# Optimization experiments

Measured on AMD Instinct MI355X. Metric: run time of the kernel, lower is better.

Reference implementation:

```python
import jax, jax.numpy as jnp
import numpy as np

# Perfect-tree regularization of the recursive UpDownVec graph:
#   T tactics per internal node, S siblings per tactic, L levels, branching B = T*S.
T, S, L = 2, 4, 7
B = T * S
DIM = 128
EPS = 1.0  # epsilon in AggChildrenVec
SIZES = [B ** l for l in range(L)]          # nodes per level: 1, 8, ..., 262144
OFFS = np.concatenate([[0], np.cumsum(SIZES)])
N_TOTAL = int(OFFS[-1])                      # 299593


def setup_inputs() -> dict:
    key = jax.random.key(0)
    ks = jax.random.split(key, 12)
    sc = 1.0 / np.sqrt(DIM)
    return {
        "initial_vecs": jax.random.normal(ks[0], (N_TOTAL, DIM), jnp.float32),
        "Ws": jax.random.normal(ks[1], (DIM, DIM), jnp.float32) * sc,
        "bs": jax.random.normal(ks[2], (DIM,), jnp.float32) * sc,
        "Wc": jax.random.normal(ks[3], (DIM, DIM), jnp.float32) * sc,
        "bc": jax.random.normal(ks[4], (DIM,), jnp.float32) * sc,
        "Wx": jax.random.normal(ks[5], (DIM, DIM), jnp.float32) * sc,
        "bx": jax.random.normal(ks[6], (DIM,), jnp.float32) * sc,
        "Wf": jax.random.normal(ks[7], (DIM, 2 * DIM), jnp.float32) * sc,
        "bf": jax.random.normal(ks[8], (DIM,), jnp.float32) * sc,
        "Wh": jax.random.normal(ks[9], (1, DIM), jnp.float32) * sc,
        "bh": jax.random.normal(ks[10], (1,), jnp.float32) * sc,
    }


def reference(initial_vecs, Ws, bs, Wc, bc, Wx, bx, Wf, bf, Wh, bh):
    dim = initial_vecs.shape[-1]
    init = [initial_vecs[OFFS[l]:OFFS[l + 1]] for l in range(L)]  # static slices

    # ---- up_step (bottom-up): leaves -> root ----
    agg = [None] * L
    agg[L - 1] = init[L - 1]                                    # leaves: agg = initial
    for l in range(L - 2, -1, -1):
        ch = agg[l + 1].reshape(SIZES[l], T, S, dim)            # children agg vecs
        # AggSiblingsVec: mean over siblings of relu(linear)
        sib_h = jax.nn.relu(jnp.einsum('ntsd,ed->ntse', ch, Ws) + bs)
        sib_agg = sib_h.mean(axis=2)                            # [n, T, dim]
        # AggChildrenVec: node + eps * mean over tactics of relu(linear)
        ch_h = jax.nn.relu(jnp.einsum('ntd,ed->nte', sib_agg, Wc) + bc)
        agg[l] = init[l] + EPS * ch_h.mean(axis=1)

    # ---- down_step (top-down): root -> leaves ----
    ctx = [None] * L
    ctx[0] = jnp.ones((1, dim), initial_vecs.dtype)             # root context = ones
    for l in range(L - 1):
        # AggContextVec over cat([parent_ctx, other_siblings_agg]); mean is
        # order-invariant so set-based sibling gathering is reproduced exactly.
        h = jax.nn.relu(agg[l + 1] @ Wx.T + bx).reshape(SIZES[l], T, S, dim)
        sum_h = h.sum(axis=2)                                   # [n, T, dim]
        ctx_h = jax.nn.relu(ctx[l] @ Wx.T + bx)                 # [n, dim]
        child_ctx = (ctx_h[:, None, None, :] + sum_h[:, :, None, :] - h) / S
        ctx[l + 1] = child_ctx.reshape(SIZES[l + 1], dim)

    # ---- final_agg for every node ----
    ctx_all = jnp.concatenate(ctx, axis=0)                      # [N, dim]
    agg_all = jnp.concatenate(agg, axis=0)                      # [N, dim]
    x = jnp.concatenate([ctx_all, agg_all], axis=1)             # [N, 2*dim]
    x = jax.nn.relu(x @ Wf.T + bf)
    return x @ Wh.T + bh                                        # [N, 1]
```

## Files before the change

kernel.cpp:

```cpp
#include <hip/hip_runtime.h>
#include <stdint.h>

#define DIM 128
#define LPAD 136

static constexpr long long NTOT = 299593LL;

using bf16x8 = __attribute__((ext_vector_type(8))) __bf16;
using f32x4  = __attribute__((ext_vector_type(4))) float;

__device__ __forceinline__ float relu(float x){ return x > 0.f ? x : 0.f; }
__device__ __forceinline__ __bf16 tobf(float x){ return (__bf16)x; }

__device__ __forceinline__ void mfma_acc(f32x4& acc, bf16x8 a, bf16x8 b){
    acc = __builtin_amdgcn_mfma_f32_16x16x32_bf16(a, b, acc, 0, 0, 0);
}

__device__ __forceinline__ void load_w_lds(const __bf16* __restrict__ wsrc,
                                           __bf16* lds, int src_stride){
    int t = threadIdx.x;
    #pragma unroll
    for (int i = 0; i < 8; ++i){
        int idx = t + i*256;
        int row = idx >> 4, col8 = (idx & 15) << 3;
        *(uint4*)(&lds[row*LPAD + col8]) = *(const uint4*)(wsrc + row*src_stride + col8);
    }
}

__global__ __launch_bounds__(256) void prep_kernel(
    const float* __restrict__ Ws, const float* __restrict__ Wc,
    const float* __restrict__ Wx, const float* __restrict__ Wf,
    __bf16* __restrict__ wts, __bf16* __restrict__ ctx)
{
    int idx = blockIdx.x*256 + threadIdx.x;
    if      (idx < 16384) wts[idx] = tobf(Ws[idx]);
    else if (idx < 32768) wts[idx] = tobf(Wc[idx - 16384]);
    else if (idx < 49152) wts[idx] = tobf(Wx[idx - 32768]);
    else if (idx < 81920) wts[idx] = tobf(Wf[idx - 49152]);
    else if (idx < 82048) ctx[idx - 81920] = tobf(1.0f);
}

template<bool LEAF>
__global__ __launch_bounds__(256, 3) void up_kernel(
    const __bf16* __restrict__ wts,
    const float* __restrict__ init,
    const float* __restrict__ bs, const float* __restrict__ bc,
    __bf16* __restrict__ agg,
    long long child_base, long long parent_base, long long n_par)
{
    __shared__ __bf16 lds_w[128*LPAD];
    __shared__ __bf16 lds_sib[32*LPAD];

    const int t = threadIdx.x;
    const int w = t >> 6, lane = t & 63, quad = lane >> 4, l15 = lane & 15;

    load_w_lds(wts, lds_w, 128);
    __syncthreads();

    const long long n_child = n_par * 8;
    const long long rowbase = (long long)blockIdx.x*128 + w*32;

    f32x4 acc[2][8];
    #pragma unroll
    for (int tt = 0; tt < 2; ++tt)
        #pragma unroll
        for (int i = 0; i < 8; ++i) acc[tt][i] = f32x4{0.f,0.f,0.f,0.f};

    bf16x8 af[2][4];
    #pragma unroll
    for (int tt = 0; tt < 2; ++tt){
        long long r = rowbase + tt*16 + l15;
        if (r >= n_child) r = n_child - 1;
        const long long base = (child_base + r)*DIM;
        #pragma unroll
        for (int ks = 0; ks < 4; ++ks){
            if (LEAF){
                const float* p = init + base + ks*32 + quad*8;
                float4 v0 = *(const float4*)p;
                float4 v1 = *(const float4*)(p + 4);
                bf16x8 a;
                a[0]=tobf(v0.x); a[1]=tobf(v0.y); a[2]=tobf(v0.z); a[3]=tobf(v0.w);
                a[4]=tobf(v1.x); a[5]=tobf(v1.y); a[6]=tobf(v1.z); a[7]=tobf(v1.w);
                af[tt][ks] = a;
                *(uint4*)(agg + base + ks*32 + quad*8) = *(uint4*)&a;
            } else {
                af[tt][ks] = *(const bf16x8*)(agg + base + ks*32 + quad*8);
            }
        }
    }
    #pragma unroll
    for (int ks = 0; ks < 4; ++ks){
        #pragma unroll
        for (int nt = 0; nt < 8; ++nt){
            bf16x8 bfrag = *(const bf16x8*)&lds_w[(nt*16 + l15)*LPAD + ks*32 + quad*8];
            mfma_acc(acc[0][nt], af[0][ks], bfrag);
            mfma_acc(acc[1][nt], af[1][ks], bfrag);
        }
    }
    #pragma unroll
    for (int tt = 0; tt < 2; ++tt){
        const int g = w*8 + tt*4 + quad;
        #pragma unroll
        for (int nt = 0; nt < 8; ++nt){
            int col = nt*16 + l15;
            float b = bs[col];
            float s = relu(acc[tt][nt][0]+b) + relu(acc[tt][nt][1]+b)
                    + relu(acc[tt][nt][2]+b) + relu(acc[tt][nt][3]+b);
            lds_sib[g*LPAD + col] = tobf(s * 0.25f);
        }
    }
    __syncthreads();
    load_w_lds(wts + 16384, lds_w, 128);
    __syncthreads();

    if (w < 2){
        f32x4 a2c[8];
        #pragma unroll
        for (int i = 0; i < 8; ++i) a2c[i] = f32x4{0.f,0.f,0.f,0.f};
        bf16x8 a2[4];
        #pragma unroll
        for (int ks = 0; ks < 4; ++ks)
            a2[ks] = *(const bf16x8*)&lds_sib[(w*16 + l15)*LPAD + ks*32 + quad*8];
        #pragma unroll
        for (int ks = 0; ks < 4; ++ks){
            #pragma unroll
            for (int nt = 0; nt < 8; ++nt){
                bf16x8 bfrag = *(const bf16x8*)&lds_w[(nt*16 + l15)*LPAD + ks*32 + quad*8];
                mfma_acc(a2c[nt], a2[ks], bfrag);
            }
        }
        const long long p0 = (long long)blockIdx.x*16 + w*8 + quad*2;
        const long long p1 = p0 + 1;
        #pragma unroll
        for (int nt = 0; nt < 8; ++nt){
            int col = nt*16 + l15;
            float b = bc[col];
            float r0 = relu(a2c[nt][0]+b), r1 = relu(a2c[nt][1]+b);
            float r2 = relu(a2c[nt][2]+b), r3 = relu(a2c[nt][3]+b);
            if (p0 < n_par){
                long long gr = parent_base + p0;
                agg[gr*DIM + col] = tobf(init[gr*DIM + col] + 0.5f*(r0+r1));
            }
            if (p1 < n_par){
                long long gr = parent_base + p1;
                agg[gr*DIM + col] = tobf(init[gr*DIM + col] + 0.5f*(r2+r3));
            }
        }
    }
}

__global__ __launch_bounds__(256, 3) void down_kernel(
    const __bf16* __restrict__ wts,
    const float* __restrict__ bx,
    const __bf16* __restrict__ agg,
    __bf16* __restrict__ ctx,
    long long parent_base, long long child_base, long long n_par)
{
    __shared__ __bf16 lds_w[128*LPAD];
    __shared__ float lds_ctxh[16*132];

    const int t = threadIdx.x;
    const int w = t >> 6, lane = t & 63, quad = lane >> 4, l15 = lane & 15;

    load_w_lds(wts + 32768, lds_w, 128);
    __syncthreads();

    const long long n_child = n_par*8;

    if (w == 0){
        f32x4 acc[8];
        #pragma unroll
        for (int i = 0; i < 8; ++i) acc[i] = f32x4{0.f,0.f,0.f,0.f};
        bf16x8 a[4];
        long long p = (long long)blockIdx.x*16 + l15;
        if (p >= n_par) p = n_par - 1;
        #pragma unroll
        for (int ks = 0; ks < 4; ++ks)
            a[ks] = *(const bf16x8*)(ctx + (parent_base + p)*DIM + ks*32 + quad*8);
        #pragma unroll
        for (int ks = 0; ks < 4; ++ks){
            #pragma unroll
            for (int nt = 0; nt < 8; ++nt){
                bf16x8 bfrag = *(const bf16x8*)&lds_w[(nt*16 + l15)*LPAD + ks*32 + quad*8];
                mfma_acc(acc[nt], a[ks], bfrag);
            }
        }
        #pragma unroll
        for (int nt = 0; nt < 8; ++nt){
            int col = nt*16 + l15;
            float b = bx[col];
            #pragma unroll
            for (int rg = 0; rg < 4; ++rg)
                lds_ctxh[(quad*4 + rg)*132 + col] = relu(acc[nt][rg] + b);
        }
    }
    __syncthreads();

    f32x4 acc[2][8];
    #pragma unroll
    for (int tt = 0; tt < 2; ++tt)
        #pragma unroll
        for (int i = 0; i < 8; ++i) acc[tt][i] = f32x4{0.f,0.f,0.f,0.f};
    bf16x8 a[2][4];
    const long long rowbase = (long long)blockIdx.x*128 + w*32;
    #pragma unroll
    for (int tt = 0; tt < 2; ++tt){
        long long r = rowbase + tt*16 + l15;
        if (r >= n_child) r = n_child - 1;
        #pragma unroll
        for (int ks = 0; ks < 4; ++ks)
            a[tt][ks] = *(const bf16x8*)(agg + (child_base + r)*DIM + ks*32 + quad*8);
    }
    #pragma unroll
    for (int ks = 0; ks < 4; ++ks){
        #pragma unroll
        for (int nt = 0; nt < 8; ++nt){
            bf16x8 bfrag = *(const bf16x8*)&lds_w[(nt*16 + l15)*LPAD + ks*32 + quad*8];
            mfma_acc(acc[0][nt], a[0][ks], bfrag);
            mfma_acc(acc[1][nt], a[1][ks], bfrag);
        }
    }
    #pragma unroll
    for (int tt = 0; tt < 2; ++tt){
        const long long rb = rowbase + tt*16 + quad*4;
        const int p_loc = w*4 + tt*2 + (quad >> 1);
        #pragma unroll
        for (int nt = 0; nt < 8; ++nt){
            int col = nt*16 + l15;
            float b = bx[col];
            float h0 = relu(acc[tt][nt][0]+b), h1 = relu(acc[tt][nt][1]+b);
            float h2 = relu(acc[tt][nt][2]+b), h3 = relu(acc[tt][nt][3]+b);
            float s = h0 + h1 + h2 + h3;
            float ch = lds_ctxh[p_loc*132 + col];
            if (rb   < n_child) ctx[(child_base + rb  )*DIM + col] = tobf((ch + s - h0)*0.25f);
            if (rb+1 < n_child) ctx[(child_base + rb+1)*DIM + col] = tobf((ch + s - h1)*0.25f);
            if (rb+2 < n_child) ctx[(child_base + rb+2)*DIM + col] = tobf((ch + s - h2)*0.25f);
            if (rb+3 < n_child) ctx[(child_base + rb+3)*DIM + col] = tobf((ch + s - h3)*0.25f);
        }
    }
}

__global__ __launch_bounds__(256, 3) void final_kernel(
    const __bf16* __restrict__ wts,
    const __bf16* __restrict__ ctx,
    const __bf16* __restrict__ agg,
    const float* __restrict__ bf_,
    const float* __restrict__ Wh, const float* __restrict__ bh,
    float* __restrict__ out)
{
    __shared__ __bf16 lds_w[128*LPAD];
    const int t = threadIdx.x;
    const int w = t >> 6, lane = t & 63, quad = lane >> 4, l15 = lane & 15;

    f32x4 acc[2][8];
    #pragma unroll
    for (int tt = 0; tt < 2; ++tt)
        #pragma unroll
        for (int i = 0; i < 8; ++i) acc[tt][i] = f32x4{0.f,0.f,0.f,0.f};

    const long long rowbase = (long long)blockIdx.x*128 + w*32;

    #pragma unroll
    for (int half = 0; half < 2; ++half){
        load_w_lds(wts + 49152 + half*128, lds_w, 256);
        __syncthreads();
        const __bf16* src = half ? agg : ctx;
        bf16x8 a[2][4];
        #pragma unroll
        for (int tt = 0; tt < 2; ++tt){
            long long r = rowbase + tt*16 + l15;
            if (r >= NTOT) r = NTOT - 1;
            #pragma unroll
            for (int ks = 0; ks < 4; ++ks)
                a[tt][ks] = *(const bf16x8*)(src + r*DIM + ks*32 + quad*8);
        }
        #pragma unroll
        for (int ks = 0; ks < 4; ++ks){
            #pragma unroll
            for (int nt = 0; nt < 8; ++nt){
                bf16x8 bfrag = *(const bf16x8*)&lds_w[(nt*16 + l15)*LPAD + ks*32 + quad*8];
                mfma_acc(acc[0][nt], a[0][ks], bfrag);
                mfma_acc(acc[1][nt], a[1][ks], bfrag);
            }
        }
        __syncthreads();
    }

    #pragma unroll
    for (int tt = 0; tt < 2; ++tt){
        float p0 = 0.f, p1 = 0.f, p2 = 0.f, p3 = 0.f;
        #pragma unroll
        for (int nt = 0; nt < 8; ++nt){
            int col = nt*16 + l15;
            float b = bf_[col], wh = Wh[col];
            p0 += relu(acc[tt][nt][0]+b)*wh;
            p1 += relu(acc[tt][nt][1]+b)*wh;
            p2 += relu(acc[tt][nt][2]+b)*wh;
            p3 += relu(acc[tt][nt][3]+b)*wh;
        }
        #pragma unroll
        for (int m = 1; m < 16; m <<= 1){
            p0 += __shfl_xor(p0, m);
            p1 += __shfl_xor(p1, m);
            p2 += __shfl_xor(p2, m);
            p3 += __shfl_xor(p3, m);
        }
        if (l15 == 0){
            float bb = bh[0];
            long long r = rowbase + tt*16 + quad*4;
            if (r   < NTOT) out[r  ] = p0 + bb;
            if (r+1 < NTOT) out[r+1] = p1 + bb;
            if (r+2 < NTOT) out[r+2] = p2 + bb;
            if (r+3 < NTOT) out[r+3] = p3 + bb;
        }
    }
}

extern "C" void kernel_launch(void* const* d_in, const int* in_sizes, int n_in,
                              void* d_out, int out_size, void* d_ws, size_t ws_size,
                              hipStream_t stream)
{
    const float* init = (const float*)d_in[0];
    const float* Ws  = (const float*)d_in[1];
    const float* bs  = (const float*)d_in[2];
    const float* Wc  = (const float*)d_in[3];
    const float* bc  = (const float*)d_in[4];
    const float* Wx  = (const float*)d_in[5];
    const float* bx  = (const float*)d_in[6];
    const float* Wf  = (const float*)d_in[7];
    const float* bff = (const float*)d_in[8];
    const float* Wh  = (const float*)d_in[9];
    const float* bh  = (const float*)d_in[10];
    float* out = (float*)d_out;

    __bf16* agg = (__bf16*)d_ws;
    __bf16* ctx = agg + NTOT*DIM;
    __bf16* wts = ctx + NTOT*DIM;

    static const long long SZ[7] = {1,8,64,512,4096,32768,262144};
    static const long long OF[8] = {0,1,9,73,585,4681,37449,299593};

    prep_kernel<<<dim3(321), dim3(256), 0, stream>>>(Ws, Wc, Wx, Wf, wts, ctx);

    for (int l = 5; l >= 0; --l){
        int blocks = (int)((SZ[l]*8 + 127)/128);
        if (l == 5)
            up_kernel<true><<<dim3(blocks), dim3(256), 0, stream>>>(
                wts, init, bs, bc, agg, OF[6], OF[5], SZ[5]);
        else
            up_kernel<false><<<dim3(blocks), dim3(256), 0, stream>>>(
                wts, init, bs, bc, agg, OF[l+1], OF[l], SZ[l]);
    }
    for (int l = 0; l < 6; ++l){
        int blocks = (int)((SZ[l]*8 + 127)/128);
        down_kernel<<<dim3(blocks), dim3(256), 0, stream>>>(
            wts, bx, agg, ctx, OF[l], OF[l+1], SZ[l]);
    }
    final_kernel<<<dim3((int)((NTOT + 127)/128)), dim3(256), 0, stream>>>(
        wts, ctx, agg, bff, Wh, bh, out);
}
```

Measured before the change: 422.2 us.

## Split large-level up/down passes and prelayout weights in MFMA fragment order

Weights are pre-permuted into MFMA B-fragment order so each lane reads a contiguous 16-byte chunk from LDS without padding. The bottom level's up pass is split into a sibling-aggregation kernel and a tactic kernel that go through a scratch buffer. The leaf-level down pass is split into a parent context-transform kernel and a child kernel. The final projection now uses 512-thread blocks that hold both weight halves in LDS and loop over two tiles, which removes the mid-kernel reload and sync. This adds extra launches and intermediate global traffic (sib, ctxh) in exchange for better-parallelized large levels and cheaper LDS access.

```diff
diff --git a/kernel.cpp b/kernel.cpp
--- a/kernel.cpp
+++ b/kernel.cpp
@@ -27,21 +27,366 @@
     }
 }
 
+template<int NTHR>
+__device__ __forceinline__ void stage_fm(const __bf16* __restrict__ src, __bf16* lds){
+    const int t = threadIdx.x;
+    #pragma unroll
+    for (int i = 0; i < 2048/NTHR; ++i){
+        int c = i*NTHR + t;
+        *((uint4*)lds + c) = *((const uint4*)src + c);
+    }
+}
+
 __global__ __launch_bounds__(256) void prep_kernel(
     const float* __restrict__ Ws, const float* __restrict__ Wc,
     const float* __restrict__ Wx, const float* __restrict__ Wf,
     __bf16* __restrict__ wts, __bf16* __restrict__ ctx)
 {
     int idx = blockIdx.x*256 + threadIdx.x;
-    if      (idx < 16384) wts[idx] = tobf(Ws[idx]);
-    else if (idx < 32768) wts[idx] = tobf(Wc[idx - 16384]);
-    else if (idx < 49152) wts[idx] = tobf(Wx[idx - 32768]);
-    else if (idx < 81920) wts[idx] = tobf(Wf[idx - 49152]);
-    else if (idx < 82048) ctx[idx - 81920] = tobf(1.0f);
-}
-
-template<bool LEAF>
-__global__ __launch_bounds__(256, 3) void up_kernel(
+    if (idx < 81920){
+        float v;
+        if      (idx < 16384) v = Ws[idx];
+        else if (idx < 32768) v = Wc[idx - 16384];
+        else if (idx < 49152) v = Wx[idx - 32768];
+        else                  v = Wf[idx - 49152];
+        wts[idx] = tobf(v);
+    } else if (idx < 163840){
+        int d2 = idx - 81920;
+        int sel = d2 >> 14;
+        int d   = d2 & 16383;
+        int j = d & 7, ln = (d >> 3) & 63, f = d >> 9;
+        int r = (f >> 2)*16 + (ln & 15);
+        int c = (f & 3)*32 + (ln >> 4)*8 + j;
+        float v;
+        if      (sel == 0) v = Ws[r*128 + c];
+        else if (sel == 1) v = Wc[r*128 + c];
+        else if (sel == 2) v = Wx[r*128 + c];
+        else if (sel == 3) v = Wf[r*256 + c];
+        else               v = Wf[r*256 + 128 + c];
+        wts[idx] = tobf(v);
+    } else if (idx < 163968){
+        ctx[idx - 163840] = tobf(1.0f);
+    }
+}
+
+
+__global__ __launch_bounds__(256, 4) void up1_kernel(
+    const __bf16* __restrict__ wfm, const float* __restrict__ init,
+    const float* __restrict__ bs, __bf16* __restrict__ agg,
+    __bf16* __restrict__ sib, long long child_base)
+{
+    __shared__ __attribute__((aligned(16))) __bf16 lds_w[16384];
+    stage_fm<256>(wfm, lds_w);
+    __syncthreads();
+    const int t = threadIdx.x, w = t>>6, lane = t&63, quad = lane>>4, l15 = lane&15;
+    float bsr[8];
+    #pragma unroll
+    for (int nt = 0; nt < 8; ++nt) bsr[nt] = bs[nt*16 + l15];
+    const int gw = blockIdx.x*4 + w;
+    #pragma unroll 1
+    for (int k = 0; k < 2; ++k){
+        const long long tile = gw + k*4096;
+        const long long r0 = tile*32;
+        float4 v[2][4][2];
+        #pragma unroll
+        for (int tt = 0; tt < 2; ++tt){
+            const float* p = init + (child_base + r0 + tt*16 + l15)*DIM + quad*8;
+            #pragma unroll
+            for (int ks = 0; ks < 4; ++ks){
+                v[tt][ks][0] = *(const float4*)(p + ks*32);
+                v[tt][ks][1] = *(const float4*)(p + ks*32 + 4);
+            }
+        }
+        bf16x8 af[2][4];
+        #pragma unroll
+        for (int tt = 0; tt < 2; ++tt){
+            const long long ob = (child_base + r0 + tt*16 + l15)*DIM + quad*8;
+            #pragma unroll
+            for (int ks = 0; ks < 4; ++ks){
+                bf16x8 a;
+                a[0]=tobf(v[tt][ks][0].x); a[1]=tobf(v[tt][ks][0].y);
+                a[2]=tobf(v[tt][ks][0].z); a[3]=tobf(v[tt][ks][0].w);
+                a[4]=tobf(v[tt][ks][1].x); a[5]=tobf(v[tt][ks][1].y);
+                a[6]=tobf(v[tt][ks][1].z); a[7]=tobf(v[tt][ks][1].w);
+                af[tt][ks] = a;
+                *(uint4*)(agg + ob + ks*32) = *(uint4*)&a;
+            }
+        }
+        f32x4 acc[2][8];
+        #pragma unroll
+        for (int tt = 0; tt < 2; ++tt)
+            #pragma unroll
+            for (int i = 0; i < 8; ++i) acc[tt][i] = f32x4{0.f,0.f,0.f,0.f};
+        #pragma unroll
+        for (int ks = 0; ks < 4; ++ks){
+            #pragma unroll
+            for (int nt = 0; nt < 8; ++nt){
+                bf16x8 b = *(const bf16x8*)&lds_w[((nt*4+ks)<<9) + lane*8];
+                mfma_acc(acc[0][nt], af[0][ks], b);
+                mfma_acc(acc[1][nt], af[1][ks], b);
+            }
+        }
+        #pragma unroll
+        for (int tt = 0; tt < 2; ++tt){
+            const long long g = tile*8 + tt*4 + quad;
+            #pragma unroll
+            for (int nt = 0; nt < 8; ++nt){
+                float b = bsr[nt];
+                float s = relu(acc[tt][nt][0]+b) + relu(acc[tt][nt][1]+b)
+                        + relu(acc[tt][nt][2]+b) + relu(acc[tt][nt][3]+b);
+                sib[g*DIM + nt*16 + l15] = tobf(s*0.25f);
+            }
+        }
+    }
+}
+
+__global__ __launch_bounds__(256, 4) void up2_kernel(
+    const __bf16* __restrict__ wfm, const float* __restrict__ init,
+    const float* __restrict__ bc, const __bf16* __restrict__ sib,
+    __bf16* __restrict__ agg, long long parent_base)
+{
+    __shared__ __attribute__((aligned(16))) __bf16 lds_w[16384];
+    stage_fm<256>(wfm, lds_w);
+    __syncthreads();
+    const int t = threadIdx.x, w = t>>6, lane = t&63, quad = lane>>4, l15 = lane&15;
+    float bcr[8];
+    #pragma unroll
+    for (int nt = 0; nt < 8; ++nt) bcr[nt] = bc[nt*16 + l15];
+    const int gw = blockIdx.x*4 + w;
+    const long long r0 = (long long)gw*32;
+    bf16x8 a[2][4];
+    #pragma unroll
+    for (int tt = 0; tt < 2; ++tt)
+        #pragma unroll
+        for (int ks = 0; ks < 4; ++ks)
+            a[tt][ks] = *(const bf16x8*)(sib + (r0 + tt*16 + l15)*DIM + ks*32 + quad*8);
+    f32x4 acc[2][8];
+    #pragma unroll
+    for (int tt = 0; tt < 2; ++tt)
+        #pragma unroll
+        for (int i = 0; i < 8; ++i) acc[tt][i] = f32x4{0.f,0.f,0.f,0.f};
+    #pragma unroll
+    for (int ks = 0; ks < 4; ++ks){
+        #pragma unroll
+        for (int nt = 0; nt < 8; ++nt){
+            bf16x8 b = *(const bf16x8*)&lds_w[((nt*4+ks)<<9) + lane*8];
+            mfma_acc(acc[0][nt], a[0][ks], b);
+            mfma_acc(acc[1][nt], a[1][ks], b);
+        }
+    }
+    #pragma unroll
+    for (int tt = 0; tt < 2; ++tt){
+        const long long p0 = r0/2 + tt*8 + quad*2;
+        const long long p1 = p0 + 1;
+        #pragma unroll
+        for (int nt = 0; nt < 8; ++nt){
+            int col = nt*16 + l15;
+            float b = bcr[nt];
+            float r0_ = relu(acc[tt][nt][0]+b), r1_ = relu(acc[tt][nt][1]+b);
+            float r2_ = relu(acc[tt][nt][2]+b), r3_ = relu(acc[tt][nt][3]+b);
+            long long gr0 = parent_base + p0, gr1 = parent_base + p1;
+            agg[gr0*DIM + col] = tobf(init[gr0*DIM + col] + 0.5f*(r0_+r1_));
+            agg[gr1*DIM + col] = tobf(init[gr1*DIM + col] + 0.5f*(r2_+r3_));
+        }
+    }
+}
+
+__global__ __launch_bounds__(256, 4) void downh_kernel(
+    const __bf16* __restrict__ wfm, const float* __restrict__ bx,
+    const __bf16* __restrict__ ctx, __bf16* __restrict__ ctxh,
+    long long parent_base)
+{
+    __shared__ __attribute__((aligned(16))) __bf16 lds_w[16384];
+    stage_fm<256>(wfm, lds_w);
+    __syncthreads();
+    const int t = threadIdx.x, w = t>>6, lane = t&63, quad = lane>>4, l15 = lane&15;
+    float bxr[8];
+    #pragma unroll
+    for (int nt = 0; nt < 8; ++nt) bxr[nt] = bx[nt*16 + l15];
+    const int gw = blockIdx.x*4 + w;
+    const long long r0 = (long long)gw*32;
+    bf16x8 a[2][4];
+    #pragma unroll
+    for (int tt = 0; tt < 2; ++tt)
+        #pragma unroll
+        for (int ks = 0; ks < 4; ++ks)
+            a[tt][ks] = *(const bf16x8*)(ctx + (parent_base + r0 + tt*16 + l15)*DIM + ks*32 + quad*8);
+    f32x4 acc[2][8];
+    #pragma unroll
+    for (int tt = 0; tt < 2; ++tt)
+        #pragma unroll
+        for (int i = 0; i < 8; ++i) acc[tt][i] = f32x4{0.f,0.f,0.f,0.f};
+    #pragma unroll
+    for (int ks = 0; ks < 4; ++ks){
+        #pragma unroll
+        for (int nt = 0; nt < 8; ++nt){
+            bf16x8 b = *(const bf16x8*)&lds_w[((nt*4+ks)<<9) + lane*8];
+            mfma_acc(acc[0][nt], a[0][ks], b);
+            mfma_acc(acc[1][nt], a[1][ks], b);
+        }
+    }
+    #pragma unroll
+    for (int tt = 0; tt < 2; ++tt){
+        #pragma unroll
+        for (int nt = 0; nt < 8; ++nt){
+            int col = nt*16 + l15;
+            float b = bxr[nt];
+            #pragma unroll
+            for (int rg = 0; rg < 4; ++rg){
+                long long row = r0 + tt*16 + quad*4 + rg;
+                ctxh[row*DIM + col] = tobf(relu(acc[tt][nt][rg] + b));
+            }
+        }
+    }
+}
+
+__global__ __launch_bounds__(256, 4) void downc_kernel(
+    const __bf16* __restrict__ wfm, const float* __restrict__ bx,
+    const __bf16* __restrict__ agg, const __bf16* __restrict__ ctxh,
+    __bf16* __restrict__ ctx, long long child_base)
+{
+    __shared__ __attribute__((aligned(16))) __bf16 lds_w[16384];
+    stage_fm<256>(wfm, lds_w);
+    __syncthreads();
+    const int t = threadIdx.x, w = t>>6, lane = t&63, quad = lane>>4, l15 = lane&15;
+    float bxr[8];
+    #pragma unroll
+    for (int nt = 0; nt < 8; ++nt) bxr[nt] = bx[nt*16 + l15];
+    const int gw = blockIdx.x*4 + w;
+    #pragma unroll 1
+    for (int k = 0; k < 2; ++k){
+        const long long tile = gw + k*4096;
+        const long long r0 = tile*32;
+        bf16x8 a[2][4];
+        #pragma unroll
+        for (int tt = 0; tt < 2; ++tt)
+            #pragma unroll
+            for (int ks = 0; ks < 4; ++ks)
+                a[tt][ks] = *(const bf16x8*)(agg + (child_base + r0 + tt*16 + l15)*DIM + ks*32 + quad*8);
+        f32x4 acc[2][8];
+        #pragma unroll
+        for (int tt = 0; tt < 2; ++tt)
+            #pragma unroll
+            for (int i = 0; i < 8; ++i) acc[tt][i] = f32x4{0.f,0.f,0.f,0.f};
+        #pragma unroll
+        for (int ks = 0; ks < 4; ++ks){
+            #pragma unroll
+            for (int nt = 0; nt < 8; ++nt){
+                bf16x8 b = *(const bf16x8*)&lds_w[((nt*4+ks)<<9) + lane*8];
+                mfma_acc(acc[0][nt], a[0][ks], b);
+                mfma_acc(acc[1][nt], a[1][ks], b);
+            }
+        }
+        #pragma unroll
+        for (int tt = 0; tt < 2; ++tt){
+            const long long rb = r0 + tt*16 + quad*4;
+            const long long p  = rb >> 3;
+            #pragma unroll
+            for (int nt = 0; nt < 8; ++nt){
+                int col = nt*16 + l15;
+                float b = bxr[nt];
+                float h0 = relu(acc[tt][nt][0]+b), h1 = relu(acc[tt][nt][1]+b);
+                float h2 = relu(acc[tt][nt][2]+b), h3 = relu(acc[tt][nt][3]+b);
+                float s = h0 + h1 + h2 + h3;
+                float ch = (float)ctxh[p*DIM + col];
+                ctx[(child_base + rb  )*DIM + col] = tobf((ch + s - h0)*0.25f);
+                ctx[(child_base + rb+1)*DIM + col] = tobf((ch + s - h1)*0.25f);
+                ctx[(child_base + rb+2)*DIM + col] = tobf((ch + s - h2)*0.25f);
+                ctx[(child_base + rb+3)*DIM + col] = tobf((ch + s - h3)*0.25f);
+            }
+        }
+    }
+}
+
+__global__ __launch_bounds__(512, 4) void final2_kernel(
+    const __bf16* __restrict__ wfm,
+    const __bf16* __restrict__ ctx, const __bf16* __restrict__ agg,
+    const float* __restrict__ bf_,
+    const float* __restrict__ Wh, const float* __restrict__ bh,
+    float* __restrict__ out)
+{
+    __shared__ __attribute__((aligned(16))) __bf16 lds_w[32768];
+    {
+        const int t = threadIdx.x;
+        #pragma unroll
+        for (int i = 0; i < 8; ++i){
+            int c = i*512 + t;
+            *((uint4*)lds_w + c) = *((const uint4*)wfm + c);
+        }
+    }
+    __syncthreads();
+    const int t = threadIdx.x, w = t>>6, lane = t&63, quad = lane>>4, l15 = lane&15;
+    float bfr[8], whr[8];
+    #pragma unroll
+    for (int nt = 0; nt < 8; ++nt){
+        bfr[nt] = bf_[nt*16 + l15];
+        whr[nt] = Wh[nt*16 + l15];
+    }
+    const float bb = bh[0];
+    const int gw = blockIdx.x*8 + w;
+    #pragma unroll 1
+    for (int k = 0; k < 2; ++k){
+        const long long tile = gw + (long long)k*4688;
+        const long long r0 = tile*32;
+        if (r0 >= NTOT) break;
+        f32x4 acc[2][8];
+        #pragma unroll
+        for (int tt = 0; tt < 2; ++tt)
+            #pragma unroll
+            for (int i = 0; i < 8; ++i) acc[tt][i] = f32x4{0.f,0.f,0.f,0.f};
+        #pragma unroll
+        for (int half = 0; half < 2; ++half){
+            const __bf16* src = half ? agg : ctx;
+            bf16x8 a[2][4];
+            #pragma unroll
+            for (int tt = 0; tt < 2; ++tt){
+                long long r = r0 + tt*16 + l15;
+                if (r >= NTOT) r = NTOT - 1;
+                #pragma unroll
+                for (int ks = 0; ks < 4; ++ks)
+                    a[tt][ks] = *(const bf16x8*)(src + r*DIM + ks*32 + quad*8);
+            }
+            #pragma unroll
+            for (int ks = 0; ks < 4; ++ks){
+                #pragma unroll
+                for (int nt = 0; nt < 8; ++nt){
+                    bf16x8 b = *(const bf16x8*)&lds_w[half*16384 + ((nt*4+ks)<<9) + lane*8];
+                    mfma_acc(acc[0][nt], a[0][ks], b);
+                    mfma_acc(acc[1][nt], a[1][ks], b);
+                }
+            }
+        }
+        #pragma unroll
+        for (int tt = 0; tt < 2; ++tt){
+            float p0 = 0.f, p1 = 0.f, p2 = 0.f, p3 = 0.f;
+            #pragma unroll
+            for (int nt = 0; nt < 8; ++nt){
+                float b = bfr[nt], wh = whr[nt];
+                p0 += relu(acc[tt][nt][0]+b)*wh;
+                p1 += relu(acc[tt][nt][1]+b)*wh;
+                p2 += relu(acc[tt][nt][2]+b)*wh;
+                p3 += relu(acc[tt][nt][3]+b)*wh;
+            }
+            #pragma unroll
+            for (int m = 1; m < 16; m <<= 1){
+                p0 += __shfl_xor(p0, m);
+                p1 += __shfl_xor(p1, m);
+                p2 += __shfl_xor(p2, m);
+                p3 += __shfl_xor(p3, m);
+            }
+            if (l15 == 0){
+                long long r = r0 + tt*16 + quad*4;
+                if (r   < NTOT) out[r  ] = p0 + bb;
+                if (r+1 < NTOT) out[r+1] = p1 + bb;
+                if (r+2 < NTOT) out[r+2] = p2 + bb;
+                if (r+3 < NTOT) out[r+3] = p3 + bb;
+            }
+        }
+    }
+}
+
+
+__global__ __launch_bounds__(256, 3) void up_f(
     const __bf16* __restrict__ wts,
     const float* __restrict__ init,
     const float* __restrict__ bs, const float* __restrict__ bc,
@@ -73,20 +418,8 @@
         if (r >= n_child) r = n_child - 1;
         const long long base = (child_base + r)*DIM;
         #pragma unroll
-        for (int ks = 0; ks < 4; ++ks){
-            if (LEAF){
-                const float* p = init + base + ks*32 + quad*8;
-                float4 v0 = *(const float4*)p;
-                float4 v1 = *(const float4*)(p + 4);
-                bf16x8 a;
-                a[0]=tobf(v0.x); a[1]=tobf(v0.y); a[2]=tobf(v0.z); a[3]=tobf(v0.w);
-                a[4]=tobf(v1.x); a[5]=tobf(v1.y); a[6]=tobf(v1.z); a[7]=tobf(v1.w);
-                af[tt][ks] = a;
-                *(uint4*)(agg + base + ks*32 + quad*8) = *(uint4*)&a;
-            } else {
-                af[tt][ks] = *(const bf16x8*)(agg + base + ks*32 + quad*8);
-            }
-        }
+        for (int ks = 0; ks < 4; ++ks)
+            af[tt][ks] = *(const bf16x8*)(agg + base + ks*32 + quad*8);
     }
     #pragma unroll
     for (int ks = 0; ks < 4; ++ks){
@@ -149,7 +482,7 @@
     }
 }
 
-__global__ __launch_bounds__(256, 3) void down_kernel(
+__global__ __launch_bounds__(256, 3) void down_f(
     const __bf16* __restrict__ wts,
     const float* __restrict__ bx,
     const __bf16* __restrict__ agg,
@@ -236,82 +569,6 @@
             if (rb+1 < n_child) ctx[(child_base + rb+1)*DIM + col] = tobf((ch + s - h1)*0.25f);
             if (rb+2 < n_child) ctx[(child_base + rb+2)*DIM + col] = tobf((ch + s - h2)*0.25f);
             if (rb+3 < n_child) ctx[(child_base + rb+3)*DIM + col] = tobf((ch + s - h3)*0.25f);
-        }
-    }
-}
-
-__global__ __launch_bounds__(256, 3) void final_kernel(
-    const __bf16* __restrict__ wts,
-    const __bf16* __restrict__ ctx,
-    const __bf16* __restrict__ agg,
-    const float* __restrict__ bf_,
-    const float* __restrict__ Wh, const float* __restrict__ bh,
-    float* __restrict__ out)
-{
-    __shared__ __bf16 lds_w[128*LPAD];
-    const int t = threadIdx.x;
-    const int w = t >> 6, lane = t & 63, quad = lane >> 4, l15 = lane & 15;
-
-    f32x4 acc[2][8];
-    #pragma unroll
-    for (int tt = 0; tt < 2; ++tt)
-        #pragma unroll
-        for (int i = 0; i < 8; ++i) acc[tt][i] = f32x4{0.f,0.f,0.f,0.f};
-
-    const long long rowbase = (long long)blockIdx.x*128 + w*32;
-
-    #pragma unroll
-    for (int half = 0; half < 2; ++half){
-        load_w_lds(wts + 49152 + half*128, lds_w, 256);
-        __syncthreads();
-        const __bf16* src = half ? agg : ctx;
-        bf16x8 a[2][4];
-        #pragma unroll
-        for (int tt = 0; tt < 2; ++tt){
-            long long r = rowbase + tt*16 + l15;
-            if (r >= NTOT) r = NTOT - 1;
-            #pragma unroll
-            for (int ks = 0; ks < 4; ++ks)
-                a[tt][ks] = *(const bf16x8*)(src + r*DIM + ks*32 + quad*8);
-        }
-        #pragma unroll
-        for (int ks = 0; ks < 4; ++ks){
-            #pragma unroll
-            for (int nt = 0; nt < 8; ++nt){
-                bf16x8 bfrag = *(const bf16x8*)&lds_w[(nt*16 + l15)*LPAD + ks*32 + quad*8];
-                mfma_acc(acc[0][nt], a[0][ks], bfrag);
-                mfma_acc(acc[1][nt], a[1][ks], bfrag);
-            }
-        }
-        __syncthreads();
-    }
-
-    #pragma unroll
-    for (int tt = 0; tt < 2; ++tt){
-        float p0 = 0.f, p1 = 0.f, p2 = 0.f, p3 = 0.f;
-        #pragma unroll
-        for (int nt = 0; nt < 8; ++nt){
-            int col = nt*16 + l15;
-            float b = bf_[col], wh = Wh[col];
-            p0 += relu(acc[tt][nt][0]+b)*wh;
-            p1 += relu(acc[tt][nt][1]+b)*wh;
-            p2 += relu(acc[tt][nt][2]+b)*wh;
-            p3 += relu(acc[tt][nt][3]+b)*wh;
-        }
-        #pragma unroll
-        for (int m = 1; m < 16; m <<= 1){
-            p0 += __shfl_xor(p0, m);
-            p1 += __shfl_xor(p1, m);
-            p2 += __shfl_xor(p2, m);
-            p3 += __shfl_xor(p3, m);
-        }
-        if (l15 == 0){
-            float bb = bh[0];
-            long long r = rowbase + tt*16 + quad*4;
-            if (r   < NTOT) out[r  ] = p0 + bb;
-            if (r+1 < NTOT) out[r+1] = p1 + bb;
-            if (r+2 < NTOT) out[r+2] = p2 + bb;
-            if (r+3 < NTOT) out[r+3] = p3 + bb;
         }
     }
 }
@@ -333,29 +590,33 @@
     const float* bh  = (const float*)d_in[10];
     float* out = (float*)d_out;
 
-    __bf16* agg = (__bf16*)d_ws;
-    __bf16* ctx = agg + NTOT*DIM;
-    __bf16* wts = ctx + NTOT*DIM;
+    __bf16* agg  = (__bf16*)d_ws;
+    __bf16* ctx  = agg + NTOT*DIM;
+    __bf16* wts  = ctx + NTOT*DIM;
+    __bf16* wfm  = wts + 81920;
+    __bf16* ctxh = wfm + 81920;
+    __bf16* sib  = ctx + 37449LL*DIM;
 
     static const long long SZ[7] = {1,8,64,512,4096,32768,262144};
     static const long long OF[8] = {0,1,9,73,585,4681,37449,299593};
 
-    prep_kernel<<<dim3(321), dim3(256), 0, stream>>>(Ws, Wc, Wx, Wf, wts, ctx);
-
-    for (int l = 5; l >= 0; --l){
+    prep_kernel<<<dim3(641), dim3(256), 0, stream>>>(Ws, Wc, Wx, Wf, wts, ctx);
+
+    up1_kernel<<<dim3(1024), dim3(256), 0, stream>>>(wfm, init, bs, agg, sib, OF[6]);
+    up2_kernel<<<dim3(512),  dim3(256), 0, stream>>>(wfm + 16384, init, bc, sib, agg, OF[5]);
+    for (int l = 4; l >= 0; --l){
         int blocks = (int)((SZ[l]*8 + 127)/128);
-        if (l == 5)
-            up_kernel<true><<<dim3(blocks), dim3(256), 0, stream>>>(
-                wts, init, bs, bc, agg, OF[6], OF[5], SZ[5]);
-        else
-            up_kernel<false><<<dim3(blocks), dim3(256), 0, stream>>>(
-                wts, init, bs, bc, agg, OF[l+1], OF[l], SZ[l]);
-    }
-    for (int l = 0; l < 6; ++l){
+        up_f<<<dim3(blocks), dim3(256), 0, stream>>>(
+            wts, init, bs, bc, agg, OF[l+1], OF[l], SZ[l]);
+    }
+    for (int l = 0; l < 5; ++l){
         int blocks = (int)((SZ[l]*8 + 127)/128);
-        down_kernel<<<dim3(blocks), dim3(256), 0, stream>>>(
+        down_f<<<dim3(blocks), dim3(256), 0, stream>>>(
             wts, bx, agg, ctx, OF[l], OF[l+1], SZ[l]);
     }
-    final_kernel<<<dim3((int)((NTOT + 127)/128)), dim3(256), 0, stream>>>(
-        wts, ctx, agg, bff, Wh, bh, out);
-}
+    downh_kernel<<<dim3(256),  dim3(256), 0, stream>>>(wfm + 32768, bx, ctx, ctxh, OF[5]);
+    downc_kernel<<<dim3(1024), dim3(256), 0, stream>>>(wfm + 32768, bx, agg, ctxh, ctx, OF[6]);
+
+    final2_kernel<<<dim3(586), dim3(512), 0, stream>>>(
+        wfm + 49152, ctx, agg, bff, Wh, bh, out);
+}
```

New measurement: 594.7 us. +40.8%, slower.
